# Kernel tuning notes

Hardware: AMD Instinct MI355X
Metric: run time of the kernel (lower is better)

The kernel has to match this reference:

```python
import math
import jax, jax.numpy as jnp
import numpy as np

D_SCALES = 4  # MSGAD d parameter


def calc_thetas(d):
    # Numeric replication of calculate_theta2 (beta-wavelet polynomial coeffs).
    # p_i(x) = (x/2)^i (1 - x/2)^(d-i) / (2 * Beta(i+1, d+1-i)); keep the d
    # lowest-order coefficients (constant .. x^{d-1}), matching the original.
    thetas = []
    for i in range(d):
        beta = math.factorial(i) * math.factorial(d - i) / math.factorial(d + 1)
        p = (np.poly1d([0.5, 0.0]) ** i) * (np.poly1d([-0.5, 1.0]) ** (d - i)) / (2.0 * beta)
        c = p.coeffs  # highest degree first, length d+1
        thetas.append([float(c[d - j]) for j in range(d)])
    return thetas

THETAS = calc_thetas(D_SCALES)


def setup_inputs() -> dict:
    key = jax.random.key(0)
    k1, k2, k3, k4 = jax.random.split(key, 4)
    N, E, IN, H = 8192, 262144, 256, 128
    in_feat = jax.random.normal(k1, (N, IN), dtype=jnp.float32)
    W = jax.random.normal(k2, (IN, H), dtype=jnp.float32) * 0.05
    b = jnp.zeros((H,), dtype=jnp.float32)
    src = jax.random.randint(k3, (E,), 0, N, dtype=jnp.int32)
    dst = jax.random.randint(k4, (E,), 0, N, dtype=jnp.int32)
    return {"in_feat": in_feat, "W": W, "b": b, "src": src, "dst": dst}


def reference(in_feat, W, b, src, dst):
    N = in_feat.shape[0]
    # Linear + LeakyReLU encoder
    h = jax.nn.leaky_relu(in_feat @ W + b, negative_slope=0.01)
    # dgl.add_self_loop
    loop = jnp.arange(N, dtype=src.dtype)
    s = jnp.concatenate([src, loop])
    d_ = jnp.concatenate([dst, loop])
    # out-degrees (with self loops), D^{-1/2} with clamp(min=1)
    deg = jax.ops.segment_sum(jnp.ones_like(s, dtype=jnp.float32), s, num_segments=N)
    dinv = jnp.maximum(deg, 1.0) ** -0.5  # [N]
    dinv = dinv[:, None]
    outs = []
    for theta in THETAS:
        feat = h
        acc = theta[0] * h
        for k in range(1, len(theta)):
            # unnormalized Laplacian: feat - D^{-1/2} A D^{-1/2} feat
            agg = jax.ops.segment_sum((feat * dinv)[s], d_, num_segments=N)
            feat = feat - agg * dinv
            acc = acc + theta[k] * feat
        outs.append(jnp.einsum('nd,md->nm', acc, acc))  # x @ x.T reconstruction
    return jnp.stack(outs)  # [d, N, N]
```

## Files before the change

kernel.cpp:

```cpp
#include <hip/hip_runtime.h>
#include <hip/hip_bf16.h>

#define N_NODES 8192
#define IN_DIM  256
#define H_DIM   128
#define N_EDGES 262144

typedef __attribute__((ext_vector_type(8))) short bf16x8;
typedef __attribute__((ext_vector_type(4))) float f32x4;
typedef __attribute__((ext_vector_type(4))) short s16x4;

static __device__ inline short bf16_hi(float x) {
    __hip_bfloat16 h = __float2bfloat16(x);
    return *(short*)&h;
}
static __device__ inline float bf16_val(short s) {
    __hip_bfloat16 h = *(__hip_bfloat16*)&s;
    return __bfloat162float(h);
}

__global__ void hist_kernel(const int* __restrict__ src, const int* __restrict__ dst,
                            int* __restrict__ degc, int* __restrict__ dstc) {
    int e = blockIdx.x * 256 + threadIdx.x;
    if (e < N_EDGES) {
        atomicAdd(&degc[src[e]], 1);
        atomicAdd(&dstc[dst[e]], 1);
    }
}

__global__ void dinv_kernel(const int* __restrict__ degc, float* __restrict__ dinv) {
    int n = blockIdx.x * 256 + threadIdx.x;
    if (n < N_NODES) dinv[n] = 1.0f / sqrtf((float)(degc[n] + 1));
}

__global__ void scan_kernel(const int* __restrict__ cnt, int* __restrict__ rowptr,
                            int* __restrict__ cursor) {
    __shared__ int buf[2][256];
    int tid = threadIdx.x;
    const int chunk = N_NODES / 256;
    int base = tid * chunk;
    int s = 0;
    for (int i = 0; i < chunk; ++i) s += cnt[base + i];
    buf[0][tid] = s;
    __syncthreads();
    int pp = 0;
    for (int off = 1; off < 256; off <<= 1) {
        buf[pp ^ 1][tid] = buf[pp][tid] + (tid >= off ? buf[pp][tid - off] : 0);
        pp ^= 1;
        __syncthreads();
    }
    if (tid == 255) rowptr[N_NODES] = buf[pp][255];
    int run = buf[pp][tid] - s;
    for (int i = 0; i < chunk; ++i) {
        rowptr[base + i] = run;
        cursor[base + i] = run;
        run += cnt[base + i];
    }
}

__global__ void fill_kernel(const int* __restrict__ src, const int* __restrict__ dst,
                            int* __restrict__ cursor, int* __restrict__ colidx) {
    int e = blockIdx.x * 256 + threadIdx.x;
    if (e < N_EDGES) {
        int p = atomicAdd(&cursor[dst[e]], 1);
        colidx[p] = src[e];
    }
}

__global__ __launch_bounds__(256) void cvtX_kernel(const f32x4* __restrict__ X,
                                                   s16x4* __restrict__ Xhi,
                                                   s16x4* __restrict__ Xlo) {
    int i = blockIdx.x * 256 + threadIdx.x;
    f32x4 x = X[i];
    s16x4 hi, lo;
#pragma unroll
    for (int j = 0; j < 4; ++j) {
        short h = bf16_hi(x[j]);
        hi[j] = h;
        lo[j] = bf16_hi(x[j] - bf16_val(h));
    }
    Xhi[i] = hi;
    Xlo[i] = lo;
}

__global__ __launch_bounds__(256) void cvtW_kernel(const float* __restrict__ W,
                                                   short* __restrict__ Wthi,
                                                   short* __restrict__ Wtlo) {
    int t = blockIdx.x * 256 + threadIdx.x;
    int k = t & 255, j = t >> 8;
    float w = W[k * H_DIM + j];
    short h = bf16_hi(w);
    Wthi[t] = h;
    Wtlo[t] = bf16_hi(w - bf16_val(h));
}

__global__ __launch_bounds__(256) void gemm_h_mfma(const short* __restrict__ Xhi,
                                                   const short* __restrict__ Xlo,
                                                   const short* __restrict__ Wthi,
                                                   const short* __restrict__ Wtlo,
                                                   const float* __restrict__ b,
                                                   const float* __restrict__ dinv,
                                                   float* __restrict__ F0,
                                                   float* __restrict__ tmp0) {
    int lane = threadIdx.x & 63;
    int w    = threadIdx.x >> 6;
    int wr = w >> 1, wc = w & 1;
    int brow = blockIdx.x * 128 + wr * 64;
    int bcol = wc * 64;
    int r16 = lane & 15;
    int kg  = lane >> 4;

    f32x4 c[4][4] = {};
    for (int kk = 0; kk < IN_DIM / 32; ++kk) {
        int koff = kk * 32 + kg * 8;
        bf16x8 ah[4], al[4], bh[4], bl[4];
#pragma unroll
        for (int m = 0; m < 4; ++m) {
            size_t off = (size_t)(brow + m * 16 + r16) * IN_DIM + koff;
            ah[m] = *(const bf16x8*)(Xhi + off);
            al[m] = *(const bf16x8*)(Xlo + off);
        }
#pragma unroll
        for (int n = 0; n < 4; ++n) {
            size_t off = (size_t)(bcol + n * 16 + r16) * IN_DIM + koff;
            bh[n] = *(const bf16x8*)(Wthi + off);
            bl[n] = *(const bf16x8*)(Wtlo + off);
        }
#pragma unroll
        for (int m = 0; m < 4; ++m)
#pragma unroll
            for (int n = 0; n < 4; ++n) {
                c[m][n] = __builtin_amdgcn_mfma_f32_16x16x32_bf16(ah[m], bh[n], c[m][n], 0, 0, 0);
                c[m][n] = __builtin_amdgcn_mfma_f32_16x16x32_bf16(ah[m], bl[n], c[m][n], 0, 0, 0);
                c[m][n] = __builtin_amdgcn_mfma_f32_16x16x32_bf16(al[m], bh[n], c[m][n], 0, 0, 0);
            }
    }
#pragma unroll
    for (int m = 0; m < 4; ++m)
#pragma unroll
        for (int n = 0; n < 4; ++n)
#pragma unroll
            for (int r = 0; r < 4; ++r) {
                int row = brow + m * 16 + kg * 4 + r;
                int col = bcol + n * 16 + r16;
                float v = c[m][n][r] + b[col];
                v = v > 0.f ? v : 0.01f * v;
                F0[(size_t)row * H_DIM + col]   = v;
                tmp0[(size_t)row * H_DIM + col] = v * dinv[row];
            }
}

__global__ __launch_bounds__(128) void prop_kernel(const float* __restrict__ Fin,
                                                   const float* __restrict__ tmpin,
                                                   float* __restrict__ Fout,
                                                   float* __restrict__ tmpout,
                                                   const float* __restrict__ dinv,
                                                   const int* __restrict__ rowptr,
                                                   const int* __restrict__ colidx) {
    int n = blockIdx.x;
    int j = threadIdx.x;
    float dv  = dinv[n];
    float fs  = Fin[(size_t)n * H_DIM + j];
    float sum = tmpin[(size_t)n * H_DIM + j];
    int beg = rowptr[n], end = rowptr[n + 1];
    int e = beg;
    for (; e + 4 <= end; e += 4) {
        int s0 = colidx[e], s1 = colidx[e + 1], s2 = colidx[e + 2], s3 = colidx[e + 3];
        float v0 = tmpin[(size_t)s0 * H_DIM + j];
        float v1 = tmpin[(size_t)s1 * H_DIM + j];
        float v2 = tmpin[(size_t)s2 * H_DIM + j];
        float v3 = tmpin[(size_t)s3 * H_DIM + j];
        sum += v0 + v1 + v2 + v3;
    }
    for (; e < end; ++e)
        sum += tmpin[(size_t)colidx[e] * H_DIM + j];
    float v = fs - sum * dv;
    Fout[(size_t)n * H_DIM + j]   = v;
    tmpout[(size_t)n * H_DIM + j] = v * dv;
}

__global__ __launch_bounds__(256) void acc_kernel(const f32x4* __restrict__ F0,
                                                  const f32x4* __restrict__ F1,
                                                  const f32x4* __restrict__ F2,
                                                  const f32x4* __restrict__ F3,
                                                  s16x4* __restrict__ accb) {
    int i = blockIdx.x * 256 + threadIdx.x;
    const size_t NH4 = (size_t)N_NODES * H_DIM / 4;
    f32x4 f0 = F0[i], f1 = F1[i], f2 = F2[i], f3 = F3[i];
    f32x4 a0 = 2.5f * f0 - 5.0f * f1 + 3.75f * f2 - 1.25f * f3;
    f32x4 a1 =           5.0f * f1 - 7.5f  * f2 + 3.75f * f3;
    f32x4 a2 =                      3.75f * f2 - 3.75f * f3;
    f32x4 a3 =                                   1.25f * f3;
    s16x4 o0, o1, o2, o3;
#pragma unroll
    for (int j = 0; j < 4; ++j) {
        o0[j] = bf16_hi(a0[j]); o1[j] = bf16_hi(a1[j]);
        o2[j] = bf16_hi(a2[j]); o3[j] = bf16_hi(a3[j]);
    }
    accb[0 * NH4 + i] = o0;
    accb[1 * NH4 + i] = o1;
    accb[2 * NH4 + i] = o2;
    accb[3 * NH4 + i] = o3;
}

__global__ __launch_bounds__(256) void out_gemm_kernel(const short* __restrict__ accb,
                                                       float* __restrict__ out) {
    int t = blockIdx.z;
    const short* A = accb + (size_t)t * N_NODES * H_DIM;
    int lane = threadIdx.x & 63;
    int w    = threadIdx.x >> 6;
    int wr = w >> 1, wc = w & 1;
    int brow = blockIdx.x * 128 + wr * 64;
    int bcol = blockIdx.y * 128 + wc * 64;
    int r16 = lane & 15;
    int kg  = lane >> 4;

    f32x4 c[4][4] = {};
    for (int kk = 0; kk < 4; ++kk) {
        int koff = kk * 32 + kg * 8;
        bf16x8 a[4], bfr[4];
#pragma unroll
        for (int m = 0; m < 4; ++m)
            a[m] = *(const bf16x8*)(A + (size_t)(brow + m * 16 + r16) * H_DIM + koff);
#pragma unroll
        for (int n = 0; n < 4; ++n)
            bfr[n] = *(const bf16x8*)(A + (size_t)(bcol + n * 16 + r16) * H_DIM + koff);
#pragma unroll
        for (int m = 0; m < 4; ++m)
#pragma unroll
            for (int n = 0; n < 4; ++n)
                c[m][n] = __builtin_amdgcn_mfma_f32_16x16x32_bf16(a[m], bfr[n], c[m][n], 0, 0, 0);
    }

    float* O = out + (size_t)t * N_NODES * N_NODES;
#pragma unroll
    for (int m = 0; m < 4; ++m)
#pragma unroll
        for (int n = 0; n < 4; ++n) {
            int col  = bcol + n * 16 + r16;
            int row0 = brow + m * 16 + kg * 4;
            __builtin_nontemporal_store(c[m][n], (f32x4*)(O + (size_t)col * N_NODES + row0));
        }
}

extern "C" void kernel_launch(void* const* d_in, const int* in_sizes, int n_in,
                              void* d_out, int out_size, void* d_ws, size_t ws_size,
                              hipStream_t stream) {
    const float* in_feat = (const float*)d_in[0];
    const float* W       = (const float*)d_in[1];
    const float* b       = (const float*)d_in[2];
    const int*   src     = (const int*)d_in[3];
    const int*   dst     = (const int*)d_in[4];
    float* out = (float*)d_out;

    char* ws = (char*)d_ws;
    const size_t NH4 = (size_t)N_NODES * H_DIM * sizeof(float);
    float* F0 = (float*)(ws + 0 * NH4);
    float* F1 = (float*)(ws + 1 * NH4);
    float* F2 = (float*)(ws + 2 * NH4);
    float* F3 = (float*)(ws + 3 * NH4);
    float* tA = (float*)(ws + 4 * NH4);
    float* tB = (float*)(ws + 5 * NH4);
    char*  accb_region = ws + 6 * NH4;
    short* accb = (short*)accb_region;
    short* Xhi = (short*)accb_region;
    short* Xlo = (short*)(accb_region + NH4);
    char* p = ws + 8 * NH4;
    int*   degc   = (int*)p;   p += 32768;
    int*   dstc   = (int*)p;   p += 32768;
    float* dinv   = (float*)p; p += 32768;
    int*   rowptr = (int*)p;   p += 33792;
    int*   cursor = (int*)p;   p += 32768;
    int*   colidx = (int*)p;   p += (size_t)N_EDGES * 4;
    short* Wthi   = (short*)p; p += 65536;
    short* Wtlo   = (short*)p;

    hipMemsetAsync(degc, 0, 65536, stream);

    hist_kernel<<<N_EDGES / 256, 256, 0, stream>>>(src, dst, degc, dstc);
    dinv_kernel<<<N_NODES / 256, 256, 0, stream>>>(degc, dinv);
    scan_kernel<<<1, 256, 0, stream>>>(dstc, rowptr, cursor);
    fill_kernel<<<N_EDGES / 256, 256, 0, stream>>>(src, dst, cursor, colidx);

    cvtX_kernel<<<(N_NODES * IN_DIM / 4) / 256, 256, 0, stream>>>((const f32x4*)in_feat,
                                                                  (s16x4*)Xhi, (s16x4*)Xlo);
    cvtW_kernel<<<(H_DIM * IN_DIM) / 256, 256, 0, stream>>>(W, Wthi, Wtlo);

    gemm_h_mfma<<<N_NODES / 128, 256, 0, stream>>>(Xhi, Xlo, Wthi, Wtlo, b, dinv, F0, tA);

    prop_kernel<<<N_NODES, 128, 0, stream>>>(F0, tA, F1, tB, dinv, rowptr, colidx);
    prop_kernel<<<N_NODES, 128, 0, stream>>>(F1, tB, F2, tA, dinv, rowptr, colidx);
    prop_kernel<<<N_NODES, 128, 0, stream>>>(F2, tA, F3, tB, dinv, rowptr, colidx);

    acc_kernel<<<(N_NODES * H_DIM / 4) / 256, 256, 0, stream>>>((const f32x4*)F0, (const f32x4*)F1,
                                                                (const f32x4*)F2, (const f32x4*)F3,
                                                                (s16x4*)accb);

    dim3 g(N_NODES / 128, N_NODES / 128, 4);
    out_gemm_kernel<<<g, 256, 0, stream>>>(accb, out);
}
```

Measured before the change: 433.7 us.

## Retile output GEMM for row-contiguous stores, shrink h-GEMM tiles, drop scaled buffers

The output GEMM is retiled so each block covers 32 rows by 512 columns, with accumulators oriented so f32x4 stores go contiguously along output rows. Nontemporal stores are replaced with plain stores. The encoder GEMM now uses 32-row tiles, which launches four times as many blocks. The prop kernel no longer reads precomputed dinv-scaled features and instead multiplies gathered neighbour values by a gathered dinv, removing the extra tmp buffers at the cost of more scattered loads.

```diff
diff --git a/kernel.cpp b/kernel.cpp
--- a/kernel.cpp
+++ b/kernel.cpp
@@ -99,27 +99,22 @@
                                                    const short* __restrict__ Wthi,
                                                    const short* __restrict__ Wtlo,
                                                    const float* __restrict__ b,
-                                                   const float* __restrict__ dinv,
-                                                   float* __restrict__ F0,
-                                                   float* __restrict__ tmp0) {
+                                                   float* __restrict__ F0) {
     int lane = threadIdx.x & 63;
     int w    = threadIdx.x >> 6;
     int wr = w >> 1, wc = w & 1;
-    int brow = blockIdx.x * 128 + wr * 64;
+    int brow = blockIdx.x * 32 + wr * 16;
     int bcol = wc * 64;
     int r16 = lane & 15;
     int kg  = lane >> 4;
 
-    f32x4 c[4][4] = {};
+    f32x4 c[4] = {};
     for (int kk = 0; kk < IN_DIM / 32; ++kk) {
         int koff = kk * 32 + kg * 8;
-        bf16x8 ah[4], al[4], bh[4], bl[4];
-#pragma unroll
-        for (int m = 0; m < 4; ++m) {
-            size_t off = (size_t)(brow + m * 16 + r16) * IN_DIM + koff;
-            ah[m] = *(const bf16x8*)(Xhi + off);
-            al[m] = *(const bf16x8*)(Xlo + off);
-        }
+        size_t aoff = (size_t)(brow + r16) * IN_DIM + koff;
+        bf16x8 ah = *(const bf16x8*)(Xhi + aoff);
+        bf16x8 al = *(const bf16x8*)(Xlo + aoff);
+        bf16x8 bh[4], bl[4];
 #pragma unroll
         for (int n = 0; n < 4; ++n) {
             size_t off = (size_t)(bcol + n * 16 + r16) * IN_DIM + koff;
@@ -127,33 +122,26 @@
             bl[n] = *(const bf16x8*)(Wtlo + off);
         }
 #pragma unroll
-        for (int m = 0; m < 4; ++m)
-#pragma unroll
-            for (int n = 0; n < 4; ++n) {
-                c[m][n] = __builtin_amdgcn_mfma_f32_16x16x32_bf16(ah[m], bh[n], c[m][n], 0, 0, 0);
-                c[m][n] = __builtin_amdgcn_mfma_f32_16x16x32_bf16(ah[m], bl[n], c[m][n], 0, 0, 0);
-                c[m][n] = __builtin_amdgcn_mfma_f32_16x16x32_bf16(al[m], bh[n], c[m][n], 0, 0, 0);
-            }
-    }
-#pragma unroll
-    for (int m = 0; m < 4; ++m)
-#pragma unroll
-        for (int n = 0; n < 4; ++n)
-#pragma unroll
-            for (int r = 0; r < 4; ++r) {
-                int row = brow + m * 16 + kg * 4 + r;
-                int col = bcol + n * 16 + r16;
-                float v = c[m][n][r] + b[col];
-                v = v > 0.f ? v : 0.01f * v;
-                F0[(size_t)row * H_DIM + col]   = v;
-                tmp0[(size_t)row * H_DIM + col] = v * dinv[row];
-            }
+        for (int n = 0; n < 4; ++n) {
+            c[n] = __builtin_amdgcn_mfma_f32_16x16x32_bf16(ah, bh[n], c[n], 0, 0, 0);
+            c[n] = __builtin_amdgcn_mfma_f32_16x16x32_bf16(ah, bl[n], c[n], 0, 0, 0);
+            c[n] = __builtin_amdgcn_mfma_f32_16x16x32_bf16(al, bh[n], c[n], 0, 0, 0);
+        }
+    }
+#pragma unroll
+    for (int n = 0; n < 4; ++n)
+#pragma unroll
+        for (int r = 0; r < 4; ++r) {
+            int row = brow + kg * 4 + r;
+            int col = bcol + n * 16 + r16;
+            float v = c[n][r] + b[col];
+            v = v > 0.f ? v : 0.01f * v;
+            F0[(size_t)row * H_DIM + col] = v;
+        }
 }
 
 __global__ __launch_bounds__(128) void prop_kernel(const float* __restrict__ Fin,
-                                                   const float* __restrict__ tmpin,
                                                    float* __restrict__ Fout,
-                                                   float* __restrict__ tmpout,
                                                    const float* __restrict__ dinv,
                                                    const int* __restrict__ rowptr,
                                                    const int* __restrict__ colidx) {
@@ -161,22 +149,23 @@
     int j = threadIdx.x;
     float dv  = dinv[n];
     float fs  = Fin[(size_t)n * H_DIM + j];
-    float sum = tmpin[(size_t)n * H_DIM + j];
+    float sum = fs * dv;
     int beg = rowptr[n], end = rowptr[n + 1];
     int e = beg;
     for (; e + 4 <= end; e += 4) {
         int s0 = colidx[e], s1 = colidx[e + 1], s2 = colidx[e + 2], s3 = colidx[e + 3];
-        float v0 = tmpin[(size_t)s0 * H_DIM + j];
-        float v1 = tmpin[(size_t)s1 * H_DIM + j];
-        float v2 = tmpin[(size_t)s2 * H_DIM + j];
-        float v3 = tmpin[(size_t)s3 * H_DIM + j];
-        sum += v0 + v1 + v2 + v3;
-    }
-    for (; e < end; ++e)
-        sum += tmpin[(size_t)colidx[e] * H_DIM + j];
-    float v = fs - sum * dv;
-    Fout[(size_t)n * H_DIM + j]   = v;
-    tmpout[(size_t)n * H_DIM + j] = v * dv;
+        float d0 = dinv[s0], d1 = dinv[s1], d2 = dinv[s2], d3 = dinv[s3];
+        float v0 = Fin[(size_t)s0 * H_DIM + j];
+        float v1 = Fin[(size_t)s1 * H_DIM + j];
+        float v2 = Fin[(size_t)s2 * H_DIM + j];
+        float v3 = Fin[(size_t)s3 * H_DIM + j];
+        sum += v0 * d0 + v1 * d1 + v2 * d2 + v3 * d3;
+    }
+    for (; e < end; ++e) {
+        int s0 = colidx[e];
+        sum += Fin[(size_t)s0 * H_DIM + j] * dinv[s0];
+    }
+    Fout[(size_t)n * H_DIM + j] = fs - sum * dv;
 }
 
 __global__ __launch_bounds__(256) void acc_kernel(const f32x4* __restrict__ F0,
@@ -209,37 +198,35 @@
     const short* A = accb + (size_t)t * N_NODES * H_DIM;
     int lane = threadIdx.x & 63;
     int w    = threadIdx.x >> 6;
-    int wr = w >> 1, wc = w & 1;
-    int brow = blockIdx.x * 128 + wr * 64;
-    int bcol = blockIdx.y * 128 + wc * 64;
+    int ib = blockIdx.y * 32;
+    int jb = blockIdx.x * 512 + w * 128;
     int r16 = lane & 15;
     int kg  = lane >> 4;
 
-    f32x4 c[4][4] = {};
+    f32x4 c[8][2] = {};
     for (int kk = 0; kk < 4; ++kk) {
         int koff = kk * 32 + kg * 8;
-        bf16x8 a[4], bfr[4];
-#pragma unroll
-        for (int m = 0; m < 4; ++m)
-            a[m] = *(const bf16x8*)(A + (size_t)(brow + m * 16 + r16) * H_DIM + koff);
-#pragma unroll
-        for (int n = 0; n < 4; ++n)
-            bfr[n] = *(const bf16x8*)(A + (size_t)(bcol + n * 16 + r16) * H_DIM + koff);
-#pragma unroll
-        for (int m = 0; m < 4; ++m)
-#pragma unroll
-            for (int n = 0; n < 4; ++n)
-                c[m][n] = __builtin_amdgcn_mfma_f32_16x16x32_bf16(a[m], bfr[n], c[m][n], 0, 0, 0);
+        bf16x8 bi[2];
+#pragma unroll
+        for (int n = 0; n < 2; ++n)
+            bi[n] = *(const bf16x8*)(A + (size_t)(ib + n * 16 + r16) * H_DIM + koff);
+#pragma unroll
+        for (int m = 0; m < 8; ++m) {
+            bf16x8 aj = *(const bf16x8*)(A + (size_t)(jb + m * 16 + r16) * H_DIM + koff);
+#pragma unroll
+            for (int n = 0; n < 2; ++n)
+                c[m][n] = __builtin_amdgcn_mfma_f32_16x16x32_bf16(aj, bi[n], c[m][n], 0, 0, 0);
+        }
     }
 
     float* O = out + (size_t)t * N_NODES * N_NODES;
 #pragma unroll
-    for (int m = 0; m < 4; ++m)
-#pragma unroll
-        for (int n = 0; n < 4; ++n) {
-            int col  = bcol + n * 16 + r16;
-            int row0 = brow + m * 16 + kg * 4;
-            __builtin_nontemporal_store(c[m][n], (f32x4*)(O + (size_t)col * N_NODES + row0));
+    for (int m = 0; m < 8; ++m)
+#pragma unroll
+        for (int n = 0; n < 2; ++n) {
+            int i  = ib + n * 16 + r16;
+            int j0 = jb + m * 16 + kg * 4;
+            *(f32x4*)(O + (size_t)i * N_NODES + j0) = c[m][n];
         }
 }
 
@@ -259,13 +246,11 @@
     float* F1 = (float*)(ws + 1 * NH4);
     float* F2 = (float*)(ws + 2 * NH4);
     float* F3 = (float*)(ws + 3 * NH4);
-    float* tA = (float*)(ws + 4 * NH4);
-    float* tB = (float*)(ws + 5 * NH4);
-    char*  accb_region = ws + 6 * NH4;
+    char*  accb_region = ws + 4 * NH4;
     short* accb = (short*)accb_region;
     short* Xhi = (short*)accb_region;
     short* Xlo = (short*)(accb_region + NH4);
-    char* p = ws + 8 * NH4;
+    char* p = ws + 6 * NH4;
     int*   degc   = (int*)p;   p += 32768;
     int*   dstc   = (int*)p;   p += 32768;
     float* dinv   = (float*)p; p += 32768;
@@ -286,16 +271,16 @@
                                                                   (s16x4*)Xhi, (s16x4*)Xlo);
     cvtW_kernel<<<(H_DIM * IN_DIM) / 256, 256, 0, stream>>>(W, Wthi, Wtlo);
 
-    gemm_h_mfma<<<N_NODES / 128, 256, 0, stream>>>(Xhi, Xlo, Wthi, Wtlo, b, dinv, F0, tA);
-
-    prop_kernel<<<N_NODES, 128, 0, stream>>>(F0, tA, F1, tB, dinv, rowptr, colidx);
-    prop_kernel<<<N_NODES, 128, 0, stream>>>(F1, tB, F2, tA, dinv, rowptr, colidx);
-    prop_kernel<<<N_NODES, 128, 0, stream>>>(F2, tA, F3, tB, dinv, rowptr, colidx);
+    gemm_h_mfma<<<N_NODES / 32, 256, 0, stream>>>(Xhi, Xlo, Wthi, Wtlo, b, F0);
+
+    prop_kernel<<<N_NODES, 128, 0, stream>>>(F0, F1, dinv, rowptr, colidx);
+    prop_kernel<<<N_NODES, 128, 0, stream>>>(F1, F2, dinv, rowptr, colidx);
+    prop_kernel<<<N_NODES, 128, 0, stream>>>(F2, F3, dinv, rowptr, colidx);
 
     acc_kernel<<<(N_NODES * H_DIM / 4) / 256, 256, 0, stream>>>((const f32x4*)F0, (const f32x4*)F1,
                                                                 (const f32x4*)F2, (const f32x4*)F3,
                                                                 (s16x4*)accb);
 
-    dim3 g(N_NODES / 128, N_NODES / 128, 4);
+    dim3 g(N_NODES / 512, N_NODES / 32, 4);
     out_gemm_kernel<<<g, 256, 0, stream>>>(accb, out);
 }
```

Measured after the change: 503.4 us. 16.1% more time.
